# Optimization experiments

Hardware: AMD Instinct MI355X
Metric: run time of the kernel (lower is better)

Reference implementation:

```python
import jax, jax.numpy as jnp
import numpy as np

# init_kwargs constants
K = 512            # out_channels (k)
THRESH = 10.0
KWTA = 16
INHIBITION_RADIUS = 0   # output spatial is 1x1; radius>0 would zero all features after 1st winner
RF_SIZE = 50
LENGTH = 2000
TIMESTEPS = 32
IN_CHANNELS = 1


def setup_inputs() -> dict:
    key = jax.random.key(0)
    k1, k2 = jax.random.split(key)
    rec_field = jax.random.normal(k1, (TIMESTEPS, IN_CHANNELS, RF_SIZE, LENGTH), dtype=jnp.float32)
    # LocalConvolution with kernel_size == input_size -> single output position;
    # weight is effectively (K, C, rf_size, length)
    weight = jax.random.normal(k2, (K, IN_CHANNELS, RF_SIZE, LENGTH), dtype=jnp.float32) * 0.02
    return {"rec_field": rec_field, "weight": weight}


def _forward(rec_field, weight):
    T = rec_field.shape[0]
    # local conv collapses to a per-timestep dense projection: (T, K)
    out = jnp.einsum('tchw,kchw->tk', rec_field, weight)
    # sf.fire: threshold potentials (keep > THRESH), spikes = sign
    pot = jnp.where(out > THRESH, out, jnp.zeros((), out.dtype))
    spike = jnp.sign(pot)
    # sf.get_k_winners (spatial dims are 1x1, work on (K,))
    nspk = spike.sum(axis=0)                                   # (K,) number of spiking timesteps
    first = jnp.clip((T - nspk).astype(jnp.int32), 0, T - 1)   # index of first spike
    values = jnp.take_along_axis(pot, first[None, :], axis=0)[0]  # potential at first spike, (K,)
    v = jnp.max(values * jnp.sign(nspk)) * T                   # large additive constant
    total = nspk * values + nspk * v                           # == truncated_pot.sum(dim=0)

    def step(tot, _):
        i = jnp.argmax(tot)
        valid = tot[i] != 0
        tot = jnp.where(valid, tot.at[i].set(0.0), tot)        # suppress winning feature
        # columnar spatial inhibition is a no-op here: output spatial size is 1x1, radius=0
        return tot, jnp.where(valid, i, -1)

    _, winners = jax.lax.scan(step, total, None, length=KWTA)  # (KWTA,) feature indices or -1
    coef = jnp.zeros((pot.shape[1],), pot.dtype).at[jnp.clip(winners, 0, None)].max(
        jnp.where(winners >= 0, 1.0, 0.0))
    # torch.mul(pot, coef).sign() ; restore (T, K, 1, 1) layout
    return jnp.sign(pot * coef[None, :])[:, :, None, None]


def reference(rec_field, weight):
    return _forward(rec_field, weight)
```

## Files before the change

### kernel.cpp

```cpp
#include <hip/hip_runtime.h>

#define RED    100000
#define TT     32
#define KF     512
#define THRESH 10.0f
#define KWTA   16

#define CHUNKS 125
#define CHUNK  800
#define RB     32
#define NSTAGE 25
#define TN     128
#define NKT    4
#define BPAD   130

template <int ATOMIC>
__global__ __launch_bounds__(256, 2)
void gemm_k(const float* __restrict__ rec, const float* __restrict__ wgt,
            float* __restrict__ dst) {
  __shared__ float Al[TT][RB];
  __shared__ float Bl[RB][BPAD];

  const int chunk = blockIdx.x;
  const int kt    = blockIdx.y;
  const int tid   = threadIdx.x;
  const int wv    = tid >> 6;
  const int ln    = tid & 63;
  const int t0    = tid >> 3;
  const int r4    = tid & 7;

  const float* ap = rec + (size_t)t0 * RED + chunk * CHUNK + r4 * 4;
  const float* bp = wgt + (size_t)(kt * TN + t0) * RED + chunk * CHUNK + r4 * 4;
  const size_t bstride = (size_t)32 * RED;

  float acc[8][2];
#pragma unroll
  for (int j = 0; j < 8; ++j) { acc[j][0] = 0.f; acc[j][1] = 0.f; }

  float4 av = *(const float4*)ap;
  float4 b0 = *(const float4*)(bp);
  float4 b1 = *(const float4*)(bp + bstride);
  float4 b2 = *(const float4*)(bp + 2 * bstride);
  float4 b3 = *(const float4*)(bp + 3 * bstride);

  for (int s = 0; s < NSTAGE; ++s) {
    __syncthreads();
    *(float4*)&Al[t0][r4 * 4] = av;
    {
      const int rr = r4 * 4;
#pragma unroll
      for (int j = 0; j < 4; ++j) {
        Bl[rr + j][t0     ] = ((const float*)&b0)[j];
        Bl[rr + j][t0 + 32] = ((const float*)&b1)[j];
        Bl[rr + j][t0 + 64] = ((const float*)&b2)[j];
        Bl[rr + j][t0 + 96] = ((const float*)&b3)[j];
      }
    }
    __syncthreads();
    if (s + 1 < NSTAGE) {
      ap += RB; bp += RB;
      av = *(const float4*)ap;
      b0 = *(const float4*)(bp);
      b1 = *(const float4*)(bp + bstride);
      b2 = *(const float4*)(bp + 2 * bstride);
      b3 = *(const float4*)(bp + 3 * bstride);
    }
#pragma unroll
    for (int r = 0; r < RB; ++r) {
      const float2 b = *(const float2*)&Bl[r][2 * ln];
#pragma unroll
      for (int j = 0; j < 8; ++j) {
        const float a = Al[wv * 8 + j][r];
        acc[j][0] = fmaf(a, b.x, acc[j][0]);
        acc[j][1] = fmaf(a, b.y, acc[j][1]);
      }
    }
  }

  if (ATOMIC) {
#pragma unroll
    for (int j = 0; j < 8; ++j) {
      const int t = wv * 8 + j;
      const int kg = kt * TN + 2 * ln;
      atomicAdd(&dst[t * KF + kg    ], acc[j][0]);
      atomicAdd(&dst[t * KF + kg + 1], acc[j][1]);
    }
  } else {
    float* p = dst + (size_t)(chunk * NKT + kt) * TT * TN;
#pragma unroll
    for (int j = 0; j < 8; ++j) {
      *(float2*)&p[(wv * 8 + j) * TN + 2 * ln] = make_float2(acc[j][0], acc[j][1]);
    }
  }
}

__global__ __launch_bounds__(256)
void reduce_k(const float* __restrict__ part, float* __restrict__ om) {
  const int i  = blockIdx.x * 256 + threadIdx.x;
  const int t  = i >> 9;
  const int k  = i & 511;
  const int kt = k >> 7;
  const int kk = k & 127;
  const float* p = part + (size_t)kt * TT * TN + (size_t)t * TN + kk;
  float s = 0.f;
  for (int c = 0; c < CHUNKS; ++c) s += p[(size_t)c * NKT * TT * TN];
  om[i] = s;
}

__global__ __launch_bounds__(512)
void kwta_k(const float* __restrict__ om, float* __restrict__ out) {
  __shared__ float tot[KF];
  __shared__ float redv[KF];
  __shared__ int   redi[KF];
  __shared__ float coef[KF];
  const int k = threadIdx.x;

  int ns = 0;
#pragma unroll
  for (int t = 0; t < TT; ++t) ns += (om[t * KF + k] > THRESH) ? 1 : 0;
  int first = TT - ns;
  if (first > TT - 1) first = TT - 1;
  float pf = om[first * KF + k];
  pf = (pf > THRESH) ? pf : 0.0f;

  redv[k] = (ns > 0) ? pf : 0.0f;
  __syncthreads();
  for (int s = 256; s >= 1; s >>= 1) {
    if (k < s) redv[k] = fmaxf(redv[k], redv[k + s]);
    __syncthreads();
  }
  const float v = redv[0] * (float)TT;

  const float t1 = (float)ns * pf;
  const float t2 = (float)ns * v;
  tot[k]  = t1 + t2;
  coef[k] = 0.0f;
  __syncthreads();

  for (int it = 0; it < KWTA; ++it) {
    redv[k] = tot[k];
    redi[k] = k;
    __syncthreads();
    for (int s = 256; s >= 1; s >>= 1) {
      if (k < s) {
        const float a = redv[k], b = redv[k + s];
        if (b > a || (b == a && redi[k + s] < redi[k])) {
          redv[k] = b; redi[k] = redi[k + s];
        }
      }
      __syncthreads();
    }
    const float mx = redv[0];
    const int   wi = redi[0];
    if (mx == 0.0f) break;
    if (k == 0) { tot[wi] = 0.0f; coef[wi] = 1.0f; }
    __syncthreads();
  }
  __syncthreads();

  for (int i = k; i < TT * KF; i += KF) {
    const int kk = i & 511;
    const float p = om[i];
    out[i] = (p > THRESH && coef[kk] != 0.0f) ? 1.0f : 0.0f;
  }
}

extern "C" void kernel_launch(void* const* d_in, const int* in_sizes, int n_in,
                              void* d_out, int out_size, void* d_ws, size_t ws_size,
                              hipStream_t stream) {
  const float* rec = (const float*)d_in[0];
  const float* wgt = (const float*)d_in[1];
  float* out = (float*)d_out;
  float* om  = (float*)d_out;
  const size_t part_bytes = (size_t)CHUNKS * NKT * TT * TN * sizeof(float);

  if (ws_size >= part_bytes) {
    float* part = (float*)d_ws;
    gemm_k<0><<<dim3(CHUNKS, NKT), 256, 0, stream>>>(rec, wgt, part);
    reduce_k<<<(TT * KF) / 256, 256, 0, stream>>>(part, om);
  } else {
    hipMemsetAsync(om, 0, (size_t)TT * KF * sizeof(float), stream);
    gemm_k<1><<<dim3(CHUNKS, NKT), 256, 0, stream>>>(rec, wgt, om);
  }
  kwta_k<<<1, 512, 0, stream>>>(om, out);
}
```

Baseline: 331.6 us.

## Keep weight tiles in registers and reduce across lanes; use wave shuffles in kWTA

The GEMM kernel no longer stages weight tiles in LDS. Each thread holds two K-columns' worth of float4 weight registers and accumulates all 32 timesteps over its 4-element reduction slot, then sums across the 8 slots with xor shuffles. This removes the transposed LDS writes of B and the matching reads, and doubles the grid in the K dimension, at the cost of 64 accumulators per thread and extra shuffle work. The kWTA kernel also replaces its LDS tree reductions with wave shuffles plus an 8-entry cross-wave pass, and the partial-sum reduce loop is unrolled.

Measured after the change: 563.0 us. 1.7x slower.

```diff
diff --git a/kernel.cpp b/kernel.cpp
--- a/kernel.cpp
+++ b/kernel.cpp
@@ -10,86 +10,82 @@
 #define CHUNK  800
 #define RB     32
 #define NSTAGE 25
-#define TN     128
-#define NKT    4
-#define BPAD   130
+#define TNK    64
+#define NKT    8
+#define KK     2
 
 template <int ATOMIC>
-__global__ __launch_bounds__(256, 2)
+__global__ __launch_bounds__(256, 4)
 void gemm_k(const float* __restrict__ rec, const float* __restrict__ wgt,
             float* __restrict__ dst) {
   __shared__ float Al[TT][RB];
-  __shared__ float Bl[RB][BPAD];
 
   const int chunk = blockIdx.x;
   const int kt    = blockIdx.y;
   const int tid   = threadIdx.x;
-  const int wv    = tid >> 6;
-  const int ln    = tid & 63;
-  const int t0    = tid >> 3;
-  const int r4    = tid & 7;
+  const int kg    = tid >> 3;
+  const int slot  = tid & 7;
 
-  const float* ap = rec + (size_t)t0 * RED + chunk * CHUNK + r4 * 4;
-  const float* bp = wgt + (size_t)(kt * TN + t0) * RED + chunk * CHUNK + r4 * 4;
+  const float* ap = rec + (size_t)kg * RED + chunk * CHUNK + slot * 4;
+  const float* bp = wgt + (size_t)(kt * TNK + kg) * RED + chunk * CHUNK + slot * 4;
   const size_t bstride = (size_t)32 * RED;
 
-  float acc[8][2];
+  float acc[TT][KK];
 #pragma unroll
-  for (int j = 0; j < 8; ++j) { acc[j][0] = 0.f; acc[j][1] = 0.f; }
+  for (int t = 0; t < TT; ++t) { acc[t][0] = 0.f; acc[t][1] = 0.f; }
 
   float4 av = *(const float4*)ap;
-  float4 b0 = *(const float4*)(bp);
+  float4 b0 = *(const float4*)bp;
   float4 b1 = *(const float4*)(bp + bstride);
-  float4 b2 = *(const float4*)(bp + 2 * bstride);
-  float4 b3 = *(const float4*)(bp + 3 * bstride);
 
   for (int s = 0; s < NSTAGE; ++s) {
     __syncthreads();
-    *(float4*)&Al[t0][r4 * 4] = av;
-    {
-      const int rr = r4 * 4;
-#pragma unroll
-      for (int j = 0; j < 4; ++j) {
-        Bl[rr + j][t0     ] = ((const float*)&b0)[j];
-        Bl[rr + j][t0 + 32] = ((const float*)&b1)[j];
-        Bl[rr + j][t0 + 64] = ((const float*)&b2)[j];
-        Bl[rr + j][t0 + 96] = ((const float*)&b3)[j];
-      }
-    }
+    *(float4*)&Al[kg][slot * 4] = av;
     __syncthreads();
+    const float4 cb0 = b0, cb1 = b1;
     if (s + 1 < NSTAGE) {
       ap += RB; bp += RB;
       av = *(const float4*)ap;
-      b0 = *(const float4*)(bp);
+      b0 = *(const float4*)bp;
       b1 = *(const float4*)(bp + bstride);
-      b2 = *(const float4*)(bp + 2 * bstride);
-      b3 = *(const float4*)(bp + 3 * bstride);
     }
 #pragma unroll
-    for (int r = 0; r < RB; ++r) {
-      const float2 b = *(const float2*)&Bl[r][2 * ln];
+    for (int t = 0; t < TT; ++t) {
+      const float4 a = *(const float4*)&Al[t][slot * 4];
+      acc[t][0] = fmaf(a.x, cb0.x, acc[t][0]);
+      acc[t][0] = fmaf(a.y, cb0.y, acc[t][0]);
+      acc[t][0] = fmaf(a.z, cb0.z, acc[t][0]);
+      acc[t][0] = fmaf(a.w, cb0.w, acc[t][0]);
+      acc[t][1] = fmaf(a.x, cb1.x, acc[t][1]);
+      acc[t][1] = fmaf(a.y, cb1.y, acc[t][1]);
+      acc[t][1] = fmaf(a.z, cb1.z, acc[t][1]);
+      acc[t][1] = fmaf(a.w, cb1.w, acc[t][1]);
+    }
+  }
+
 #pragma unroll
-      for (int j = 0; j < 8; ++j) {
-        const float a = Al[wv * 8 + j][r];
-        acc[j][0] = fmaf(a, b.x, acc[j][0]);
-        acc[j][1] = fmaf(a, b.y, acc[j][1]);
-      }
+  for (int m = 1; m <= 4; m <<= 1) {
+#pragma unroll
+    for (int t = 0; t < TT; ++t) {
+      acc[t][0] += __shfl_xor(acc[t][0], m, 64);
+      acc[t][1] += __shfl_xor(acc[t][1], m, 64);
     }
   }
 
   if (ATOMIC) {
 #pragma unroll
-    for (int j = 0; j < 8; ++j) {
-      const int t = wv * 8 + j;
-      const int kg = kt * TN + 2 * ln;
-      atomicAdd(&dst[t * KF + kg    ], acc[j][0]);
-      atomicAdd(&dst[t * KF + kg + 1], acc[j][1]);
+    for (int j = 0; j < 4; ++j) {
+      const int t = slot * 4 + j;
+      atomicAdd(&dst[t * KF + kt * TNK + kg     ], acc[t][0]);
+      atomicAdd(&dst[t * KF + kt * TNK + kg + 32], acc[t][1]);
     }
   } else {
-    float* p = dst + (size_t)(chunk * NKT + kt) * TT * TN;
+    float* p = dst + (size_t)(chunk * NKT + kt) * TT * TNK;
 #pragma unroll
-    for (int j = 0; j < 8; ++j) {
-      *(float2*)&p[(wv * 8 + j) * TN + 2 * ln] = make_float2(acc[j][0], acc[j][1]);
+    for (int j = 0; j < 4; ++j) {
+      const int t = slot * 4 + j;
+      p[t * TNK + kg     ] = acc[t][0];
+      p[t * TNK + kg + 32] = acc[t][1];
     }
   }
 }
@@ -99,21 +95,25 @@
   const int i  = blockIdx.x * 256 + threadIdx.x;
   const int t  = i >> 9;
   const int k  = i & 511;
-  const int kt = k >> 7;
-  const int kk = k & 127;
-  const float* p = part + (size_t)kt * TT * TN + (size_t)t * TN + kk;
+  const int kt = k >> 6;
+  const int kk = k & 63;
+  const float* p = part + (size_t)kt * TT * TNK + (size_t)t * TNK + kk;
   float s = 0.f;
-  for (int c = 0; c < CHUNKS; ++c) s += p[(size_t)c * NKT * TT * TN];
+#pragma unroll 5
+  for (int c = 0; c < CHUNKS; ++c) s += p[(size_t)c * NKT * TT * TNK];
   om[i] = s;
 }
 
 __global__ __launch_bounds__(512)
 void kwta_k(const float* __restrict__ om, float* __restrict__ out) {
   __shared__ float tot[KF];
-  __shared__ float redv[KF];
-  __shared__ int   redi[KF];
   __shared__ float coef[KF];
-  const int k = threadIdx.x;
+  __shared__ float wmax[8];
+  __shared__ int   widx[8];
+  __shared__ float bflag;
+  const int k    = threadIdx.x;
+  const int lane = k & 63;
+  const int wv   = k >> 6;
 
   int ns = 0;
 #pragma unroll
@@ -123,13 +123,15 @@
   float pf = om[first * KF + k];
   pf = (pf > THRESH) ? pf : 0.0f;
 
-  redv[k] = (ns > 0) ? pf : 0.0f;
+  float m = (ns > 0) ? pf : 0.0f;
+#pragma unroll
+  for (int off = 1; off <= 32; off <<= 1) m = fmaxf(m, __shfl_xor(m, off, 64));
+  if (lane == 0) wmax[wv] = m;
   __syncthreads();
-  for (int s = 256; s >= 1; s >>= 1) {
-    if (k < s) redv[k] = fmaxf(redv[k], redv[k + s]);
-    __syncthreads();
-  }
-  const float v = redv[0] * (float)TT;
+  float v = wmax[0];
+#pragma unroll
+  for (int w = 1; w < 8; ++w) v = fmaxf(v, wmax[w]);
+  v *= (float)TT;
 
   const float t1 = (float)ns * pf;
   const float t2 = (float)ns * v;
@@ -138,23 +140,26 @@
   __syncthreads();
 
   for (int it = 0; it < KWTA; ++it) {
-    redv[k] = tot[k];
-    redi[k] = k;
+    float val = tot[k];
+    int   idx = k;
+#pragma unroll
+    for (int off = 1; off <= 32; off <<= 1) {
+      const float ov = __shfl_xor(val, off, 64);
+      const int   oi = __shfl_xor(idx, off, 64);
+      if (ov > val || (ov == val && oi < idx)) { val = ov; idx = oi; }
+    }
+    if (lane == 0) { wmax[wv] = val; widx[wv] = idx; }
     __syncthreads();
-    for (int s = 256; s >= 1; s >>= 1) {
-      if (k < s) {
-        const float a = redv[k], b = redv[k + s];
-        if (b > a || (b == a && redi[k + s] < redi[k])) {
-          redv[k] = b; redi[k] = redi[k + s];
-        }
-      }
-      __syncthreads();
+    if (k == 0) {
+      float bv = wmax[0]; int bi = widx[0];
+#pragma unroll
+      for (int w = 1; w < 8; ++w)
+        if (wmax[w] > bv || (wmax[w] == bv && widx[w] < bi)) { bv = wmax[w]; bi = widx[w]; }
+      if (bv != 0.0f) { tot[bi] = 0.0f; coef[bi] = 1.0f; bflag = 1.0f; }
+      else            { bflag = 0.0f; }
     }
-    const float mx = redv[0];
-    const int   wi = redi[0];
-    if (mx == 0.0f) break;
-    if (k == 0) { tot[wi] = 0.0f; coef[wi] = 1.0f; }
     __syncthreads();
+    if (bflag == 0.0f) break;
   }
   __syncthreads();
 
@@ -172,7 +177,7 @@
   const float* wgt = (const float*)d_in[1];
   float* out = (float*)d_out;
   float* om  = (float*)d_out;
-  const size_t part_bytes = (size_t)CHUNKS * NKT * TT * TN * sizeof(float);
+  const size_t part_bytes = (size_t)CHUNKS * NKT * TT * TNK * sizeof(float);
 
   if (ws_size >= part_bytes) {
     float* part = (float*)d_ws;
```
